# Kernel optimization log

Hardware: AMD Instinct MI355X
Metric: run time of the kernel (lower is better)

The kernel has to match this reference:

```python
import jax, jax.numpy as jnp
import numpy as np

D_EMB = 1024
D_HEAD = 64
B = 4
T = 4096


def setup_inputs() -> dict:
    key = jax.random.key(0)
    kx, kk, kq, kv = jax.random.split(key, 4)
    s = 1.0 / np.sqrt(D_EMB)  # torch Linear default init scale (uniform bound)
    x = jax.random.normal(kx, (B, T, D_EMB), dtype=jnp.float32)
    Wk = jax.random.uniform(kk, (D_HEAD, D_EMB), jnp.float32, -s, s)
    Wq = jax.random.uniform(kq, (D_HEAD, D_EMB), jnp.float32, -s, s)
    Wv = jax.random.uniform(kv, (D_HEAD, D_EMB), jnp.float32, -s, s)
    return {"x": x, "Wk": Wk, "Wq": Wq, "Wv": Wv}


def reference(x, Wk, Wq, Wv):
    # x: (B, T, d_emb); W*: (d_head, d_emb) -- torch Linear stores (out, in)
    k = jnp.einsum('bte,he->bth', x, Wk)
    q = jnp.einsum('bte,he->bth', x, Wq)
    v = jnp.einsum('bte,he->bth', x, Wv)
    scale = D_HEAD ** (-0.5)
    a = jnp.einsum('bth,bsh->bts', q, k) * scale  # (B, T, T)
    Tlen = x.shape[-2]
    causal = jnp.tril(jnp.ones((Tlen, Tlen), dtype=bool))
    a = jnp.where(causal, a, -jnp.inf)
    a = jax.nn.softmax(a, axis=-1)
    return jnp.einsum('bts,bsh->bth', a, v)  # (B, T, d_head)
```

## Files before the change

kernel.cpp:

```cpp
#include <hip/hip_runtime.h>
#include <hip/hip_bf16.h>

#define D_EMB 1024
#define T_LEN 4096
#define NTASK2 544

typedef short short8 __attribute__((ext_vector_type(8)));
typedef float f32x4 __attribute__((ext_vector_type(4)));
typedef float f32x16 __attribute__((ext_vector_type(16)));
typedef float float4v __attribute__((ext_vector_type(4)));

__device__ __forceinline__ unsigned short f32_to_bf16(float f) {
    union { float f; unsigned int u; } c; c.f = f;
    unsigned int u = c.u;
    return (unsigned short)((u + 0x7FFFu + ((u >> 16) & 1u)) >> 16);
}
__device__ __forceinline__ float bf16_to_f32(unsigned short v) {
    union { unsigned int u; float f; } c; c.u = ((unsigned int)v) << 16;
    return c.f;
}
__device__ __forceinline__ unsigned cvtpk_bf16(float a, float b) {
    unsigned r;
    asm("v_cvt_pk_bf16_f32 %0, %1, %2" : "=v"(r) : "v"(a), "v"(b));
    return r;
}
__device__ __forceinline__ float xhalf_max(float x) {
    return fmaxf(x, __shfl_xor(x, 32));
}
__device__ __forceinline__ float xhalf_add(float x) {
    return x + __shfl_xor(x, 32);
}
__device__ __forceinline__ void gl_lds16(const void* g, void* l) {
    __builtin_amdgcn_global_load_lds(
        (const __attribute__((address_space(1))) unsigned int*)(g),
        (__attribute__((address_space(3))) unsigned int*)(l), 16, 0, 0);
}

#define QSCALE (0.125f * 1.44269504f)

__global__ __launch_bounds__(256) void convert_w(const float* __restrict__ Wk,
                                                 const float* __restrict__ Wq,
                                                 const float* __restrict__ Wv,
                                                 unsigned short* __restrict__ Wb) {
    int e = (blockIdx.x * 256 + threadIdx.x) * 8;
    const float* src;
    if (e < 65536) src = Wk + e;
    else if (e < 131072) src = Wq + (e - 65536);
    else src = Wv + (e - 131072);
    float4v a0 = *(const float4v*)src;
    float4v a1 = *(const float4v*)(src + 4);
    short8 r;
    r[0] = (short)f32_to_bf16(a0[0]); r[1] = (short)f32_to_bf16(a0[1]);
    r[2] = (short)f32_to_bf16(a0[2]); r[3] = (short)f32_to_bf16(a0[3]);
    r[4] = (short)f32_to_bf16(a1[0]); r[5] = (short)f32_to_bf16(a1[1]);
    r[6] = (short)f32_to_bf16(a1[2]); r[7] = (short)f32_to_bf16(a1[3]);
    int row = e >> 10;
    int dst = e ^ ((row & 7) << 3);
    *(short8*)(Wb + dst) = r;
}

__global__ __launch_bounds__(256, 2) void qkv_proj(const float* __restrict__ x,
                                                   const unsigned short* __restrict__ Wb,
                                                   unsigned short* __restrict__ Kb,
                                                   unsigned short* __restrict__ Qb,
                                                   unsigned short* __restrict__ Vt) {
    __shared__ __attribute__((aligned(16))) unsigned short Wsl[2][12288];

    int tid = threadIdx.x;
    int lane = tid & 63, wave = tid >> 6;
    int lo = lane & 15, hi = lane >> 4;
    int rg = wave >> 1, nh = wave & 1;
    int row0 = blockIdx.x * 32;

    const float* xp = x + (size_t)(row0 + rg * 16 + lo) * D_EMB + hi * 8;

    f32x4 acc[6];
#pragma unroll
    for (int i = 0; i < 6; i++) acc[i] = (f32x4){0.f, 0.f, 0.f, 0.f};

    float4v xa0 = *(const float4v*)(xp);
    float4v xa1 = *(const float4v*)(xp + 4);
    float4v xa2 = *(const float4v*)(xp + 32);
    float4v xa3 = *(const float4v*)(xp + 36);
    float4v xb0 = *(const float4v*)(xp + 64);
    float4v xb1 = *(const float4v*)(xp + 68);
    float4v xb2 = *(const float4v*)(xp + 96);
    float4v xb3 = *(const float4v*)(xp + 100);

#pragma unroll
    for (int j = 0; j < 6; j++) {
        int unit = j * 4 + wave;
        int u = unit * 64 + lane;
        gl_lds16(Wb + (size_t)(u >> 3) * D_EMB + (u & 7) * 8, &Wsl[0][unit * 512]);
    }
    __syncthreads();

    int buf = 0;
    int xorm = (lo & 7) << 4;
    int rowbase = nh * 96 + lo;

    for (int kt = 0; kt < 16; kt++) {
        int ktn = (kt < 14) ? kt + 2 : 15;
        const float* pn = xp + ktn * 64;
        float4v xc0 = *(const float4v*)(pn);
        float4v xc1 = *(const float4v*)(pn + 4);
        float4v xc2 = *(const float4v*)(pn + 32);
        float4v xc3 = *(const float4v*)(pn + 36);

        if (kt < 15) {
            int k0n = (kt + 1) * 64;
#pragma unroll
            for (int j = 0; j < 6; j++) {
                int unit = j * 4 + wave;
                int u = unit * 64 + lane;
                gl_lds16(Wb + (size_t)(u >> 3) * D_EMB + k0n + (u & 7) * 8,
                         &Wsl[buf ^ 1][unit * 512]);
            }
        }

        short8 af[2];
        {
            union { unsigned u[4]; short8 s; } c;
            c.u[0] = cvtpk_bf16(xa0[0], xa0[1]);
            c.u[1] = cvtpk_bf16(xa0[2], xa0[3]);
            c.u[2] = cvtpk_bf16(xa1[0], xa1[1]);
            c.u[3] = cvtpk_bf16(xa1[2], xa1[3]);
            af[0] = c.s;
            c.u[0] = cvtpk_bf16(xa2[0], xa2[1]);
            c.u[1] = cvtpk_bf16(xa2[2], xa2[3]);
            c.u[2] = cvtpk_bf16(xa3[0], xa3[1]);
            c.u[3] = cvtpk_bf16(xa3[2], xa3[3]);
            af[1] = c.s;
        }

        const char* sb = (const char*)&Wsl[buf][0];
#pragma unroll
        for (int i = 0; i < 6; i++) {
            int row = rowbase + i * 16;
#pragma unroll
            for (int ks = 0; ks < 2; ks++) {
                short8 bfrag = *(const short8*)(sb + row * 128 + ((ks * 64 + hi * 16) ^ xorm));
                acc[i] = __builtin_amdgcn_mfma_f32_16x16x32_bf16(af[ks], bfrag, acc[i], 0, 0, 0);
            }
        }
        __syncthreads();
        buf ^= 1;
        xa0 = xb0; xa1 = xb1; xa2 = xb2; xa3 = xb3;
        xb0 = xc0; xb1 = xc1; xb2 = xc2; xb3 = xc3;
    }

#pragma unroll
    for (int i = 0; i < 6; i++) {
        int n = nh * 6 + i;
#pragma unroll
        for (int r = 0; r < 4; r++) {
            int grow = row0 + rg * 16 + hi * 4 + r;
            float val = acc[i][r];
            if (n < 4) {
                Kb[(size_t)grow * 64 + n * 16 + lo] = f32_to_bf16(val);
            } else if (n < 8) {
                Qb[(size_t)grow * 64 + (n - 4) * 16 + lo] = f32_to_bf16(val * QSCALE);
            } else {
                int bb = grow >> 12;
                Vt[((size_t)bb * 64 + (n - 8) * 16 + lo) * T_LEN + (grow & 4095)] = f32_to_bf16(val);
            }
        }
    }
}

__global__ __launch_bounds__(64, 2) void attn(const unsigned short* __restrict__ Qb,
                                              const unsigned short* __restrict__ Kb,
                                              const unsigned short* __restrict__ Vt,
                                              unsigned short* __restrict__ Opart,
                                              float* __restrict__ Mpart,
                                              float* __restrict__ Lpart) {
    int lane = threadIdx.x;
    int q32 = lane & 31;
    int hi = lane >> 5;
    unsigned lin = blockIdx.x;
    int b = lin & 3;
    int s = (int)(((lin >> 3) << 1) | ((lin >> 2) & 1));

    int k = 16, rem = s;
    while (rem >= 4 * k) { rem -= 4 * k; k--; }
    int ti = rem / k;
    int st = 4 * k - 1 - ti;
    int c = rem - ti * k;

    int u0 = c * 8;
    int u1 = min(u0 + 8, 2 * st + 2);
    int ta = 2 * st, tb = ta + 1;
    int qrowA = 64 * st + q32;
    int qrowB = qrowA + 32;

    size_t base = (size_t)b * T_LEN;

    short8 qfa[4], qfb[4];
    const unsigned short* qpa = Qb + (base + qrowA) * 64 + hi * 8;
    const unsigned short* qpb = Qb + (base + qrowB) * 64 + hi * 8;
#pragma unroll
    for (int d = 0; d < 4; d++) {
        qfa[d] = *(const short8*)(qpa + d * 16);
        qfb[d] = *(const short8*)(qpb + d * 16);
    }

    size_t vbase = ((size_t)b * 64 + q32) * T_LEN;
    f32x16 oA0 = {0.f}, oA1 = {0.f}, oB0 = {0.f}, oB1 = {0.f};
    float mA = -3e38f, lA = 0.f, mB = -3e38f, lB = 0.f;

    for (int u = u0; u < u1; ++u) {
        const unsigned short* kp = Kb + (base + u * 32 + q32) * 64 + hi * 8;
        short8 kc0 = *(const short8*)kp;
        short8 kc1 = *(const short8*)(kp + 16);
        short8 kc2 = *(const short8*)(kp + 32);
        short8 kc3 = *(const short8*)(kp + 48);
        const unsigned short* vp = Vt + vbase + u * 32 + hi * 8;
        short8 vc0 = *(const short8*)vp;
        short8 vc1 = *(const short8*)(vp + 16);
        short8 vc2 = *(const short8*)(vp + 32 * T_LEN);
        short8 vc3 = *(const short8*)(vp + 32 * T_LEN + 16);

        f32x16 sa = {0.f}, sb = {0.f};
        sa = __builtin_amdgcn_mfma_f32_32x32x16_bf16(kc0, qfa[0], sa, 0, 0, 0);
        sb = __builtin_amdgcn_mfma_f32_32x32x16_bf16(kc0, qfb[0], sb, 0, 0, 0);
        sa = __builtin_amdgcn_mfma_f32_32x32x16_bf16(kc1, qfa[1], sa, 0, 0, 0);
        sb = __builtin_amdgcn_mfma_f32_32x32x16_bf16(kc1, qfb[1], sb, 0, 0, 0);
        sa = __builtin_amdgcn_mfma_f32_32x32x16_bf16(kc2, qfa[2], sa, 0, 0, 0);
        sb = __builtin_amdgcn_mfma_f32_32x32x16_bf16(kc2, qfb[2], sb, 0, 0, 0);
        sa = __builtin_amdgcn_mfma_f32_32x32x16_bf16(kc3, qfa[3], sa, 0, 0, 0);
        sb = __builtin_amdgcn_mfma_f32_32x32x16_bf16(kc3, qfb[3], sb, 0, 0, 0);

        if (u >= ta) {
#pragma unroll
            for (int r = 0; r < 16; ++r) {
                int key = 32 * u + (r & 3) + 8 * (r >> 2) + 4 * hi;
                sa[r] = (key <= qrowA) ? sa[r] : -3e38f;
                if (u == tb) sb[r] = (key <= qrowB) ? sb[r] : -3e38f;
            }
        }

        float a0 = fmaxf(fmaxf(sa[0], sa[1]), sa[2]);
        float a1 = fmaxf(fmaxf(sa[3], sa[4]), sa[5]);
        float a2 = fmaxf(fmaxf(sa[6], sa[7]), sa[8]);
        float a3 = fmaxf(fmaxf(sa[9], sa[10]), sa[11]);
        float a4 = fmaxf(fmaxf(sa[12], sa[13]), sa[14]);
        float mxA = fmaxf(fmaxf(fmaxf(a0, a1), fmaxf(a2, a3)), fmaxf(a4, sa[15]));
        float b0 = fmaxf(fmaxf(sb[0], sb[1]), sb[2]);
        float b1 = fmaxf(fmaxf(sb[3], sb[4]), sb[5]);
        float b2 = fmaxf(fmaxf(sb[6], sb[7]), sb[8]);
        float b3 = fmaxf(fmaxf(sb[9], sb[10]), sb[11]);
        float b4 = fmaxf(fmaxf(sb[12], sb[13]), sb[14]);
        float mxB = fmaxf(fmaxf(fmaxf(b0, b1), fmaxf(b2, b3)), fmaxf(b4, sb[15]));
        mxA = xhalf_max(mxA);
        mxB = xhalf_max(mxB);

        float grow = fmaxf(mxA - mA, mxB - mB);
        if (__any(grow > 8.0f)) {
            float mnA = fmaxf(mA, mxA);
            float alA = exp2f(mA - mnA);
            mA = mnA; lA *= alA;
            float mnB = fmaxf(mB, mxB);
            float alB = exp2f(mB - mnB);
            mB = mnB; lB *= alB;
#pragma unroll
            for (int r = 0; r < 16; ++r) {
                oA0[r] *= alA; oA1[r] *= alA;
                oB0[r] *= alB; oB1[r] *= alB;
            }
        }

#pragma unroll
        for (int r = 0; r < 16; ++r) {
            sa[r] = exp2f(sa[r] - mA);
            sb[r] = exp2f(sb[r] - mB);
        }
        float yA = ((sa[0] + sa[8]) + (sa[4] + sa[12])) + ((sa[1] + sa[9]) + (sa[5] + sa[13]))
                 + ((sa[2] + sa[10]) + (sa[6] + sa[14])) + ((sa[3] + sa[11]) + (sa[7] + sa[15]));
        float yB = ((sb[0] + sb[8]) + (sb[4] + sb[12])) + ((sb[1] + sb[9]) + (sb[5] + sb[13]))
                 + ((sb[2] + sb[10]) + (sb[6] + sb[14])) + ((sb[3] + sb[11]) + (sb[7] + sb[15]));
        lA += xhalf_add(yA);
        lB += xhalf_add(yB);

        unsigned pa0 = cvtpk_bf16(sa[0],  sa[1]);
        unsigned pa1 = cvtpk_bf16(sa[2],  sa[3]);
        unsigned pa2 = cvtpk_bf16(sa[4],  sa[5]);
        unsigned pa3 = cvtpk_bf16(sa[6],  sa[7]);
        unsigned pa4 = cvtpk_bf16(sa[8],  sa[9]);
        unsigned pa5 = cvtpk_bf16(sa[10], sa[11]);
        unsigned pa6 = cvtpk_bf16(sa[12], sa[13]);
        unsigned pa7 = cvtpk_bf16(sa[14], sa[15]);
        unsigned pb0 = cvtpk_bf16(sb[0],  sb[1]);
        unsigned pb1 = cvtpk_bf16(sb[2],  sb[3]);
        unsigned pb2 = cvtpk_bf16(sb[4],  sb[5]);
        unsigned pb3 = cvtpk_bf16(sb[6],  sb[7]);
        unsigned pb4 = cvtpk_bf16(sb[8],  sb[9]);
        unsigned pb5 = cvtpk_bf16(sb[10], sb[11]);
        unsigned pb6 = cvtpk_bf16(sb[12], sb[13]);
        unsigned pb7 = cvtpk_bf16(sb[14], sb[15]);
        asm("v_permlane32_swap_b32 %0, %1" : "+v"(pa0), "+v"(pa2));
        asm("v_permlane32_swap_b32 %0, %1" : "+v"(pa1), "+v"(pa3));
        asm("v_permlane32_swap_b32 %0, %1" : "+v"(pa4), "+v"(pa6));
        asm("v_permlane32_swap_b32 %0, %1" : "+v"(pa5), "+v"(pa7));
        asm("v_permlane32_swap_b32 %0, %1" : "+v"(pb0), "+v"(pb2));
        asm("v_permlane32_swap_b32 %0, %1" : "+v"(pb1), "+v"(pb3));
        asm("v_permlane32_swap_b32 %0, %1" : "+v"(pb4), "+v"(pb6));
        asm("v_permlane32_swap_b32 %0, %1" : "+v"(pb5), "+v"(pb7));
        union U8 { unsigned u[4]; short8 s; };
        U8 fA0; fA0.u[0] = pa0; fA0.u[1] = pa1; fA0.u[2] = pa2; fA0.u[3] = pa3;
        U8 fA1; fA1.u[0] = pa4; fA1.u[1] = pa5; fA1.u[2] = pa6; fA1.u[3] = pa7;
        U8 fB0; fB0.u[0] = pb0; fB0.u[1] = pb1; fB0.u[2] = pb2; fB0.u[3] = pb3;
        U8 fB1; fB1.u[0] = pb4; fB1.u[1] = pb5; fB1.u[2] = pb6; fB1.u[3] = pb7;

        oA0 = __builtin_amdgcn_mfma_f32_32x32x16_bf16(vc0, fA0.s, oA0, 0, 0, 0);
        oB0 = __builtin_amdgcn_mfma_f32_32x32x16_bf16(vc0, fB0.s, oB0, 0, 0, 0);
        oA0 = __builtin_amdgcn_mfma_f32_32x32x16_bf16(vc1, fA1.s, oA0, 0, 0, 0);
        oB0 = __builtin_amdgcn_mfma_f32_32x32x16_bf16(vc1, fB1.s, oB0, 0, 0, 0);
        oA1 = __builtin_amdgcn_mfma_f32_32x32x16_bf16(vc2, fA0.s, oA1, 0, 0, 0);
        oB1 = __builtin_amdgcn_mfma_f32_32x32x16_bf16(vc2, fB0.s, oB1, 0, 0, 0);
        oA1 = __builtin_amdgcn_mfma_f32_32x32x16_bf16(vc3, fA1.s, oA1, 0, 0, 0);
        oB1 = __builtin_amdgcn_mfma_f32_32x32x16_bf16(vc3, fB1.s, oB1, 0, 0, 0);
    }

    int slotA = (b * NTASK2 + s) * 2;
    size_t tbA = ((size_t)slotA * 32 + q32) * 64;
    size_t tbB = ((size_t)(slotA + 1) * 32 + q32) * 64;
#pragma unroll
    for (int hb = 0; hb < 2; hb++) {
#pragma unroll
        for (int g = 0; g < 4; g++) {
            float eA0 = hb ? oA1[4 * g] : oA0[4 * g];
            float eA1 = hb ? oA1[4 * g + 1] : oA0[4 * g + 1];
            float eA2 = hb ? oA1[4 * g + 2] : oA0[4 * g + 2];
            float eA3 = hb ? oA1[4 * g + 3] : oA0[4 * g + 3];
            float eB0 = hb ? oB1[4 * g] : oB0[4 * g];
            float eB1 = hb ? oB1[4 * g + 1] : oB0[4 * g + 1];
            float eB2 = hb ? oB1[4 * g + 2] : oB0[4 * g + 2];
            float eB3 = hb ? oB1[4 * g + 3] : oB0[4 * g + 3];
            int h0 = hb * 32 + g * 8 + hi * 4;
            *reinterpret_cast<uint2*>(Opart + tbA + h0) =
                make_uint2(cvtpk_bf16(eA0, eA1), cvtpk_bf16(eA2, eA3));
            *reinterpret_cast<uint2*>(Opart + tbB + h0) =
                make_uint2(cvtpk_bf16(eB0, eB1), cvtpk_bf16(eB2, eB3));
        }
    }
    if (lane < 32) {
        Mpart[slotA * 32 + q32] = mA;
        Lpart[slotA * 32 + q32] = lA;
        Mpart[(slotA + 1) * 32 + q32] = mB;
        Lpart[(slotA + 1) * 32 + q32] = lB;
    }
}

__global__ __launch_bounds__(256) void attn_merge(const unsigned short* __restrict__ Opart,
                                                  const float* __restrict__ Mpart,
                                                  const float* __restrict__ Lpart,
                                                  float* __restrict__ out) {
    int tid = threadIdx.x;
    int g = blockIdx.x * 64 + (tid >> 2);
    int h0 = (tid & 3) * 16;
    int b = g >> 12, t = g & 4095;
    int tile32 = t >> 5, r32 = t & 31;
    int st = tile32 >> 1, member = tile32 & 1;
    int k = (st >> 2) + 1;
    int sbase = 4 * (136 - ((k * (k + 1)) >> 1));
    int ti = 4 * k - 1 - st;
    int s0 = sbase + ti * k;
    int slot0 = (b * NTASK2 + s0) * 2 + member;

    float mm = -3e38f;
    for (int i = 0; i < k; i++) mm = fmaxf(mm, Mpart[(slot0 + 2 * i) * 32 + r32]);
    float ll = 0.f;
    float acc[16];
#pragma unroll
    for (int e = 0; e < 16; e++) acc[e] = 0.f;
    for (int i = 0; i < k; i++) {
        int slot = slot0 + 2 * i;
        float a = exp2f(Mpart[slot * 32 + r32] - mm);
        ll += a * Lpart[slot * 32 + r32];
        const unsigned short* op = Opart + ((size_t)slot * 32 + r32) * 64 + h0;
        short8 v0 = *(const short8*)op;
        short8 v1 = *(const short8*)(op + 8);
#pragma unroll
        for (int e = 0; e < 8; e++) {
            acc[e]     += a * bf16_to_f32((unsigned short)v0[e]);
            acc[8 + e] += a * bf16_to_f32((unsigned short)v1[e]);
        }
    }
    float inv = 1.f / ll;
    float* dst = out + (size_t)g * 64 + h0;
#pragma unroll
    for (int e = 0; e < 16; e++) dst[e] = acc[e] * inv;
}

extern "C" void kernel_launch(void* const* d_in, const int* in_sizes, int n_in,
                              void* d_out, int out_size, void* d_ws, size_t ws_size,
                              hipStream_t stream) {
    (void)in_sizes; (void)n_in; (void)out_size; (void)ws_size;
    const float* x  = (const float*)d_in[0];
    const float* Wk = (const float*)d_in[1];
    const float* Wq = (const float*)d_in[2];
    const float* Wv = (const float*)d_in[3];
    float* out = (float*)d_out;

    unsigned short* Wb = (unsigned short*)d_ws;
    unsigned short* Kb = Wb + 196608;
    unsigned short* Qb = Kb + 1048576;
    unsigned short* Vt = Qb + 1048576;
    unsigned short* Opart = Vt + 1048576;
    float* Mpart = (float*)(Opart + (size_t)4 * NTASK2 * 2 * 32 * 64);
    float* Lpart = Mpart + 4 * NTASK2 * 2 * 32;

    hipLaunchKernelGGL(convert_w, dim3(96), dim3(256), 0, stream, Wk, Wq, Wv, Wb);
    hipLaunchKernelGGL(qkv_proj, dim3(512), dim3(256), 0, stream, x, Wb, Kb, Qb, Vt);
    hipLaunchKernelGGL(attn, dim3(4 * NTASK2), dim3(64), 0, stream, Qb, Kb, Vt, Opart, Mpart, Lpart);
    hipLaunchKernelGGL(attn_merge, dim3(256), dim3(256), 0, stream, Opart, Mpart, Lpart, out);
}
```

Baseline: 81.81 us.

## Rewrite QKV projection to stream weights directly without LDS staging

The QKV projection drops the double-buffered LDS staging of bf16 weights and the swizzled weight layout. Each wave now reads its weight fragments straight from global memory (L2-resident), and each block handles 16 rows instead of 32, so twice as many blocks are launched at higher occupancy. This removes LDS traffic and block-wide barriers but gives up explicit prefetch, which leaves the kernel relying on the cache and on occupancy to hide the latency of x and weight loads. Every wave re-reads its x rows, and weight reuse per block is lower.

```diff
diff --git a/kernel.cpp b/kernel.cpp
--- a/kernel.cpp
+++ b/kernel.cpp
@@ -29,11 +29,6 @@
 }
 __device__ __forceinline__ float xhalf_add(float x) {
     return x + __shfl_xor(x, 32);
-}
-__device__ __forceinline__ void gl_lds16(const void* g, void* l) {
-    __builtin_amdgcn_global_load_lds(
-        (const __attribute__((address_space(1))) unsigned int*)(g),
-        (__attribute__((address_space(3))) unsigned int*)(l), 16, 0, 0);
 }
 
 #define QSCALE (0.125f * 1.44269504f)
@@ -54,108 +49,51 @@
     r[2] = (short)f32_to_bf16(a0[2]); r[3] = (short)f32_to_bf16(a0[3]);
     r[4] = (short)f32_to_bf16(a1[0]); r[5] = (short)f32_to_bf16(a1[1]);
     r[6] = (short)f32_to_bf16(a1[2]); r[7] = (short)f32_to_bf16(a1[3]);
-    int row = e >> 10;
-    int dst = e ^ ((row & 7) << 3);
-    *(short8*)(Wb + dst) = r;
-}
-
-__global__ __launch_bounds__(256, 2) void qkv_proj(const float* __restrict__ x,
+    *(short8*)(Wb + e) = r;
+}
+
+__global__ __launch_bounds__(256, 8) void qkv_proj(const float* __restrict__ x,
                                                    const unsigned short* __restrict__ Wb,
                                                    unsigned short* __restrict__ Kb,
                                                    unsigned short* __restrict__ Qb,
                                                    unsigned short* __restrict__ Vt) {
-    __shared__ __attribute__((aligned(16))) unsigned short Wsl[2][12288];
-
     int tid = threadIdx.x;
     int lane = tid & 63, wave = tid >> 6;
     int lo = lane & 15, hi = lane >> 4;
-    int rg = wave >> 1, nh = wave & 1;
-    int row0 = blockIdx.x * 32;
-
-    const float* xp = x + (size_t)(row0 + rg * 16 + lo) * D_EMB + hi * 8;
-
-    f32x4 acc[6];
-#pragma unroll
-    for (int i = 0; i < 6; i++) acc[i] = (f32x4){0.f, 0.f, 0.f, 0.f};
-
-    float4v xa0 = *(const float4v*)(xp);
-    float4v xa1 = *(const float4v*)(xp + 4);
-    float4v xa2 = *(const float4v*)(xp + 32);
-    float4v xa3 = *(const float4v*)(xp + 36);
-    float4v xb0 = *(const float4v*)(xp + 64);
-    float4v xb1 = *(const float4v*)(xp + 68);
-    float4v xb2 = *(const float4v*)(xp + 96);
-    float4v xb3 = *(const float4v*)(xp + 100);
-
-#pragma unroll
-    for (int j = 0; j < 6; j++) {
-        int unit = j * 4 + wave;
-        int u = unit * 64 + lane;
-        gl_lds16(Wb + (size_t)(u >> 3) * D_EMB + (u & 7) * 8, &Wsl[0][unit * 512]);
-    }
-    __syncthreads();
-
-    int buf = 0;
-    int xorm = (lo & 7) << 4;
-    int rowbase = nh * 96 + lo;
-
-    for (int kt = 0; kt < 16; kt++) {
-        int ktn = (kt < 14) ? kt + 2 : 15;
-        const float* pn = xp + ktn * 64;
-        float4v xc0 = *(const float4v*)(pn);
-        float4v xc1 = *(const float4v*)(pn + 4);
-        float4v xc2 = *(const float4v*)(pn + 32);
-        float4v xc3 = *(const float4v*)(pn + 36);
-
-        if (kt < 15) {
-            int k0n = (kt + 1) * 64;
-#pragma unroll
-            for (int j = 0; j < 6; j++) {
-                int unit = j * 4 + wave;
-                int u = unit * 64 + lane;
-                gl_lds16(Wb + (size_t)(u >> 3) * D_EMB + k0n + (u & 7) * 8,
-                         &Wsl[buf ^ 1][unit * 512]);
-            }
-        }
-
-        short8 af[2];
-        {
-            union { unsigned u[4]; short8 s; } c;
-            c.u[0] = cvtpk_bf16(xa0[0], xa0[1]);
-            c.u[1] = cvtpk_bf16(xa0[2], xa0[3]);
-            c.u[2] = cvtpk_bf16(xa1[0], xa1[1]);
-            c.u[3] = cvtpk_bf16(xa1[2], xa1[3]);
-            af[0] = c.s;
-            c.u[0] = cvtpk_bf16(xa2[0], xa2[1]);
-            c.u[1] = cvtpk_bf16(xa2[2], xa2[3]);
-            c.u[2] = cvtpk_bf16(xa3[0], xa3[1]);
-            c.u[3] = cvtpk_bf16(xa3[2], xa3[3]);
-            af[1] = c.s;
-        }
-
-        const char* sb = (const char*)&Wsl[buf][0];
-#pragma unroll
-        for (int i = 0; i < 6; i++) {
-            int row = rowbase + i * 16;
-#pragma unroll
-            for (int ks = 0; ks < 2; ks++) {
-                short8 bfrag = *(const short8*)(sb + row * 128 + ((ks * 64 + hi * 16) ^ xorm));
-                acc[i] = __builtin_amdgcn_mfma_f32_16x16x32_bf16(af[ks], bfrag, acc[i], 0, 0, 0);
-            }
-        }
-        __syncthreads();
-        buf ^= 1;
-        xa0 = xb0; xa1 = xb1; xa2 = xb2; xa3 = xb3;
-        xb0 = xc0; xb1 = xc1; xb2 = xc2; xb3 = xc3;
-    }
-
-#pragma unroll
-    for (int i = 0; i < 6; i++) {
-        int n = nh * 6 + i;
+    int row0 = blockIdx.x * 16;
+
+    const float* xp = x + (size_t)(row0 + lo) * D_EMB + hi * 8;
+    const unsigned short* wp = Wb + (size_t)(wave * 48 + lo) * D_EMB + hi * 8;
+
+    f32x4 acc0 = (f32x4){0.f, 0.f, 0.f, 0.f};
+    f32x4 acc1 = (f32x4){0.f, 0.f, 0.f, 0.f};
+    f32x4 acc2 = (f32x4){0.f, 0.f, 0.f, 0.f};
+
+#pragma unroll 8
+    for (int kt = 0; kt < 32; kt++) {
+        float4v a0 = *(const float4v*)(xp + kt * 32);
+        float4v a1 = *(const float4v*)(xp + kt * 32 + 4);
+        short8 b0 = *(const short8*)(wp + kt * 32);
+        short8 b1 = *(const short8*)(wp + 16 * D_EMB + kt * 32);
+        short8 b2 = *(const short8*)(wp + 32 * D_EMB + kt * 32);
+        union { unsigned u[4]; short8 s; } c;
+        c.u[0] = cvtpk_bf16(a0[0], a0[1]);
+        c.u[1] = cvtpk_bf16(a0[2], a0[3]);
+        c.u[2] = cvtpk_bf16(a1[0], a1[1]);
+        c.u[3] = cvtpk_bf16(a1[2], a1[3]);
+        acc0 = __builtin_amdgcn_mfma_f32_16x16x32_bf16(c.s, b0, acc0, 0, 0, 0);
+        acc1 = __builtin_amdgcn_mfma_f32_16x16x32_bf16(c.s, b1, acc1, 0, 0, 0);
+        acc2 = __builtin_amdgcn_mfma_f32_16x16x32_bf16(c.s, b2, acc2, 0, 0, 0);
+    }
+
+    f32x4 accs[3] = {acc0, acc1, acc2};
+#pragma unroll
+    for (int i = 0; i < 3; i++) {
+        int n = wave * 3 + i;
 #pragma unroll
         for (int r = 0; r < 4; r++) {
-            int grow = row0 + rg * 16 + hi * 4 + r;
-            float val = acc[i][r];
+            int grow = row0 + hi * 4 + r;
+            float val = accs[i][r];
             if (n < 4) {
                 Kb[(size_t)grow * 64 + n * 16 + lo] = f32_to_bf16(val);
             } else if (n < 8) {
@@ -411,7 +349,7 @@
     float* Lpart = Mpart + 4 * NTASK2 * 2 * 32;
 
     hipLaunchKernelGGL(convert_w, dim3(96), dim3(256), 0, stream, Wk, Wq, Wv, Wb);
-    hipLaunchKernelGGL(qkv_proj, dim3(512), dim3(256), 0, stream, x, Wb, Kb, Qb, Vt);
+    hipLaunchKernelGGL(qkv_proj, dim3(1024), dim3(256), 0, stream, x, Wb, Kb, Qb, Vt);
     hipLaunchKernelGGL(attn, dim3(4 * NTASK2), dim3(64), 0, stream, Qb, Kb, Vt, Opart, Mpart, Lpart);
     hipLaunchKernelGGL(attn_merge, dim3(256), dim3(256), 0, stream, Opart, Mpart, Lpart, out);
 }
```

Result: slower. 127.5 us (+55.9%).
